# Kernel tuning notes

Hardware: AMD Instinct MI355X
Metric: run time of the kernel (lower is better)

The kernel has to match this reference:

```python
import jax, jax.numpy as jnp
import numpy as np

ANG = float(np.deg2rad(20.0))  # max rotation/shear angle (rad)
MAX_T = 6.0                    # max translation (pixels)


def _affine_mats(random, Wc, Hc):
    # Faithful to TCR.forward: note tx==ty and r==hx==hy since all use the same `random`.
    tx = (2.0 * MAX_T) * random - MAX_T
    ty = (2.0 * MAX_T) * random - MAX_T
    r = (2.0 * ANG) * random - ANG
    z = jnp.ones_like(random)          # max_z == min_z == 1.0
    hx = (2.0 * ANG) * random - ANG
    hy = (2.0 * ANG) * random - ANG
    a = hx - r
    b = hy + r
    chx, chy = jnp.cos(hx), jnp.cos(hy)
    T11 = z * jnp.cos(a) / chx
    T12 = z * jnp.sin(a) / chx
    T13 = (Wc * chx - Wc * z * jnp.cos(a) + 2 * tx * z * jnp.cos(a)
           - Hc * z * jnp.sin(a) + 2 * ty * z * jnp.sin(a)) / (2 * chx)
    T21 = z * jnp.sin(b) / chy
    T22 = z * jnp.cos(b) / chy
    T23 = (Hc * chy - Wc * z * jnp.cos(b) + 2 * ty * z * jnp.cos(b)
           - Wc * z * jnp.sin(b) + 2 * tx * z * jnp.sin(b)) / (2 * chy)
    row0 = jnp.stack([T11, T12, T13], axis=-1)
    row1 = jnp.stack([T21, T22, T23], axis=-1)
    return jnp.stack([row0, row1], axis=1)  # (B, 2, 3)


def _bilinear_sample(img, sx, sy):
    # img (B,C,H,W); sx,sy (B,H,W) source pixel coords; zeros padding (grid_sample semantics).
    B, C, H, W = img.shape
    x0f = jnp.floor(sx)
    y0f = jnp.floor(sy)
    x0 = x0f.astype(jnp.int32)
    y0 = y0f.astype(jnp.int32)
    wx = (sx - x0f)[:, None]  # (B,1,H,W)
    wy = (sy - y0f)[:, None]
    imgf = img.reshape(B, C, H * W)

    def gather(yi, xi):
        valid = (yi >= 0) & (yi < H) & (xi >= 0) & (xi < W)
        idx = jnp.clip(yi, 0, H - 1) * W + jnp.clip(xi, 0, W - 1)
        idx = jnp.broadcast_to(idx.reshape(B, 1, H * W), (B, C, H * W))
        v = jnp.take_along_axis(imgf, idx, axis=2).reshape(B, C, H, W)
        return v * valid[:, None, :, :].astype(img.dtype)

    v00 = gather(y0, x0)
    v01 = gather(y0, x0 + 1)
    v10 = gather(y0 + 1, x0)
    v11 = gather(y0 + 1, x0 + 1)
    return (v00 * (1 - wx) * (1 - wy) + v01 * wx * (1 - wy)
            + v10 * (1 - wx) * wy + v11 * wx * wy)


def _warp_affine(img, T):
    # kornia.warp_affine with align_corners=True reduces to: dst(x,y) = src(T^{-1} [x,y,1]).
    B, C, H, W = img.shape
    a, b, c = T[:, 0, 0], T[:, 0, 1], T[:, 0, 2]
    d, e, f = T[:, 1, 0], T[:, 1, 1], T[:, 1, 2]
    det = a * e - b * d
    ia, ib = e / det, -b / det
    id_, ie = -d / det, a / det
    ic = -(ia * c + ib * f)
    if_ = -(id_ * c + ie * f)
    ys, xs = jnp.meshgrid(jnp.arange(H, dtype=img.dtype),
                          jnp.arange(W, dtype=img.dtype), indexing='ij')
    bc = lambda v: v[:, None, None]  # (B,) -> (B,1,1)
    sx = bc(ia) * xs + bc(ib) * ys + bc(ic)  # (B,H,W)
    sy = bc(id_) * xs + bc(ie) * ys + bc(if_)
    return _bilinear_sample(img, sx, sy)


def setup_inputs() -> dict:
    key = jax.random.key(0)
    k1, k2 = jax.random.split(key)
    img = jax.random.normal(k1, (64, 3, 256, 256), dtype=jnp.float32)
    random = jax.random.uniform(k2, (64,), dtype=jnp.float32)
    return {"img": img, "random": random}


def reference(img, random):
    # Original uses Wc = img.shape[2], Hc = img.shape[3] (NCHW); square so equivalent.
    Wc = img.shape[2]
    Hc = img.shape[3]
    T = _affine_mats(random, float(Wc), float(Hc))
    return _warp_affine(img, T)
```

## Files before the change

kernel.cpp:

```cpp
#include <hip/hip_runtime.h>
#include <math.h>

#define BATCH 64
#define CH 3
#define IMH 256
#define IMW 256
#define HW (IMH * IMW)
#define NXCD 8

#define NRMAX 184
#define XW 36
#define XW4 9
#define NQ (NRMAX * XW4)
#define NIT 7

#define AS1 __attribute__((address_space(1)))
#define AS3 __attribute__((address_space(3)))

__device__ __forceinline__ int clampi(int v, int lo, int hi) {
    return min(max(v, lo), hi);
}

__global__ __launch_bounds__(256, 6) void TCR_52536039964687_warp(
    const float* __restrict__ img,
    const float* __restrict__ rnd,
    float* __restrict__ out) {
    __shared__ float4 lds4[NQ];
    float* lds = (float*)lds4;

    int w = blockIdx.x;
    int xcd = w & (NXCD - 1);
    unsigned t = (unsigned)w >> 3;
    unsigned islot = t / 48u;
    unsigned rem = t - islot * 48u;
    int b = ((int)islot << 3) | xcd;
    int ch = (int)(rem >> 4);
    int tile = (int)(rem & 15u);
    int X0 = (tile & 7) << 5;
    int Y0 = (tile >> 3) << 7;

    int tid = threadIdx.x;
    int dx = tid & 31;
    int qy = tid >> 5;

    const float r = rnd[b];
    const float ANG  = 0.34906585039886590f;
    const float ANG2 = 0.69813170079773179f;
    const float Wc = (float)IMH;
    const float Hc = (float)IMW;

    float tx  = 12.0f * r - 6.0f;
    float ty  = tx;
    float rho = ANG2 * r - ANG;

    float s = __sinf(rho);
    float c = __cosf(rho);
    float cb = 2.f * c * c - 1.f;
    float sb = 2.f * s * c;
    float rcb = 1.f / cb;

    float ic  = 0.5f * Wc * (1.f - c) - tx;
    float id_ = -sb * c * rcb;
    float ie  = c * rcb;
    float P   = 0.5f * (Wc * c - Wc + 2.f * tx);
    float Q   = 0.5f * (Hc * c - Wc * cb + 2.f * ty * cb - Wc * sb + 2.f * tx * sb);
    float if_ = (sb * P - Q) * rcb;

    float X0f = (float)X0, X1f = (float)(X0 + 31);
    float Y0f = (float)Y0, Y1f = (float)(Y0 + 127);
    float sxlo = fmaf(c, X0f, ic);
    int lxmin = clampi((int)floorf(sxlo), 0, IMW - 2);
    int axlo = lxmin & ~3;

    float g0 = fmaf(ie, Y0f, if_);
    float g1 = fmaf(ie, Y1f, if_);
    float syA = fmaf(id_, X0f, g0), syB = fmaf(id_, X1f, g0);
    float syC = fmaf(id_, X0f, g1), syD = fmaf(id_, X1f, g1);
    float symin = fminf(fminf(syA, syB), fminf(syC, syD));
    float symax = fmaxf(fmaxf(syA, syB), fmaxf(syC, syD));
    int rlo = clampi((int)floorf(symin), 0, IMH - 1);
    int rhi = clampi((int)floorf(symax) + 1, 0, IMH - 1);
    int NR = rhi - rlo + 1;
    int nq = NR * XW4;

    {
        const float* cbase = img + (size_t)b * CH * HW + ch * HW;
        #pragma unroll
        for (int it = 0; it < NIT; ++it) {
            int e = tid + it * 256;
            if (e < nq) {
                unsigned row = (unsigned)e / XW4;
                int q = e - (int)row * XW4;
                int gq = min(axlo + 4 * q, IMW - 4);
                const float* gp = cbase + (rlo + (int)row) * IMW + gq;
                __builtin_amdgcn_global_load_lds((const AS1 void*)gp,
                                                 (AS3 void*)&lds4[e], 16, 0, 0);
            }
        }
    }

    float fx = (float)(X0 + dx);
    float sx = fmaf(c, fx, ic);
    float x0f = floorf(sx);
    int x0 = (int)x0f;
    float wx = sx - x0f;
    int lx = clampi(x0, 0, IMW - 2);
    float wl = (x0 == lx) ? (1.f - wx) : ((x0 == lx - 1) ? wx : 0.f);
    float wh = (x0 == lx) ? wx : ((x0 == lx + 1) ? (1.f - wx) : 0.f);
    int px = lx - axlo;

    int   a01[16];
    float wy0[16], wy1[16];
    #pragma unroll
    for (int k = 0; k < 16; ++k) {
        float fy = (float)(Y0 + qy + 8 * k);
        float sy = fmaf(id_, fx, fmaf(ie, fy, if_));
        float y0f = floorf(sy);
        int y0 = (int)y0f;
        int y1 = y0 + 1;
        float wy = sy - y0f;
        wy0[k] = ((y0 >= 0) & (y0 < IMH)) ? (1.f - wy) : 0.f;
        wy1[k] = ((y1 >= 0) & (y1 < IMH)) ? wy : 0.f;
        int a0 = (clampi(y0, 0, IMH - 1) - rlo) * XW + px;
        int a1 = (clampi(y1, 0, IMH - 1) - rlo) * XW + px;
        a01[k] = a0 | (a1 << 16);
    }

    __syncthreads();

    float* obase = out + (size_t)b * CH * HW + ch * HW
                 + (Y0 + qy) * IMW + X0 + dx;
    #pragma unroll
    for (int k = 0; k < 16; ++k) {
        int a0 = a01[k] & 0xffff;
        int a1 = a01[k] >> 16;
        float l00 = lds[a0], l01 = lds[a0 + 1];
        float l10 = lds[a1], l11 = lds[a1 + 1];
        float v = (l00 * wl + l01 * wh) * wy0[k]
                + (l10 * wl + l11 * wh) * wy1[k];
        __builtin_nontemporal_store(v, obase + 8 * k * IMW);
    }
}

extern "C" void kernel_launch(void* const* d_in, const int* in_sizes, int n_in,
                              void* d_out, int out_size, void* d_ws, size_t ws_size,
                              hipStream_t stream) {
    const float* img = (const float*)d_in[0];
    const float* rnd = (const float*)d_in[1];
    float* out = (float*)d_out;
    (void)d_ws; (void)ws_size;

    hipLaunchKernelGGL(TCR_52536039964687_warp, dim3(BATCH * 16 * CH), dim3(256),
                       0, stream, img, rnd, out);
}
```

Baseline: 23.96 us.

## Switch to full-height column bands with float4 stores per thread

Each block now covers a full-height 32-column band instead of a 32x128 tile. It stages all 256 source rows of the 36-wide column window into LDS, with no computed row range, and halves the grid. Each thread produces 4 adjacent output pixels per row and writes them with a single float4 store instead of scalar nontemporal stores. This reduces per-block overhead and duplicated halo rows, at the cost of larger LDS use, lower occupancy (launch bounds 4) and more LDS loads of rows that may never be read.

```diff
diff --git a/kernel.cpp b/kernel.cpp
--- a/kernel.cpp
+++ b/kernel.cpp
@@ -8,11 +8,10 @@
 #define HW (IMH * IMW)
 #define NXCD 8
 
-#define NRMAX 184
 #define XW 36
 #define XW4 9
-#define NQ (NRMAX * XW4)
-#define NIT 7
+#define NQ (IMH * XW4)
+#define NIT 9
 
 #define AS1 __attribute__((address_space(1)))
 #define AS3 __attribute__((address_space(3)))
@@ -21,7 +20,7 @@
     return min(max(v, lo), hi);
 }
 
-__global__ __launch_bounds__(256, 6) void TCR_52536039964687_warp(
+__global__ __launch_bounds__(256, 4) void TCR_52536039964687_warp(
     const float* __restrict__ img,
     const float* __restrict__ rnd,
     float* __restrict__ out) {
@@ -31,17 +30,16 @@
     int w = blockIdx.x;
     int xcd = w & (NXCD - 1);
     unsigned t = (unsigned)w >> 3;
-    unsigned islot = t / 48u;
-    unsigned rem = t - islot * 48u;
+    unsigned islot = t / 24u;
+    unsigned rem = t - islot * 24u;
     int b = ((int)islot << 3) | xcd;
-    int ch = (int)(rem >> 4);
-    int tile = (int)(rem & 15u);
-    int X0 = (tile & 7) << 5;
-    int Y0 = (tile >> 3) << 7;
+    int ch = (int)(rem >> 3);
+    int band = (int)(rem & 7u);
+    int X0 = band << 5;
 
     int tid = threadIdx.x;
-    int dx = tid & 31;
-    int qy = tid >> 5;
+    int cg = tid & 7;
+    int qy = tid >> 3;
 
     const float r = rnd[b];
     const float ANG  = 0.34906585039886590f;
@@ -66,79 +64,66 @@
     float Q   = 0.5f * (Hc * c - Wc * cb + 2.f * ty * cb - Wc * sb + 2.f * tx * sb);
     float if_ = (sb * P - Q) * rcb;
 
-    float X0f = (float)X0, X1f = (float)(X0 + 31);
-    float Y0f = (float)Y0, Y1f = (float)(Y0 + 127);
-    float sxlo = fmaf(c, X0f, ic);
+    float sxlo = fmaf(c, (float)X0, ic);
     int lxmin = clampi((int)floorf(sxlo), 0, IMW - 2);
     int axlo = lxmin & ~3;
 
-    float g0 = fmaf(ie, Y0f, if_);
-    float g1 = fmaf(ie, Y1f, if_);
-    float syA = fmaf(id_, X0f, g0), syB = fmaf(id_, X1f, g0);
-    float syC = fmaf(id_, X0f, g1), syD = fmaf(id_, X1f, g1);
-    float symin = fminf(fminf(syA, syB), fminf(syC, syD));
-    float symax = fmaxf(fmaxf(syA, syB), fmaxf(syC, syD));
-    int rlo = clampi((int)floorf(symin), 0, IMH - 1);
-    int rhi = clampi((int)floorf(symax) + 1, 0, IMH - 1);
-    int NR = rhi - rlo + 1;
-    int nq = NR * XW4;
+    const float* cbase = img + (size_t)b * CH * HW + ch * HW;
 
-    {
-        const float* cbase = img + (size_t)b * CH * HW + ch * HW;
-        #pragma unroll
-        for (int it = 0; it < NIT; ++it) {
-            int e = tid + it * 256;
-            if (e < nq) {
-                unsigned row = (unsigned)e / XW4;
-                int q = e - (int)row * XW4;
-                int gq = min(axlo + 4 * q, IMW - 4);
-                const float* gp = cbase + (rlo + (int)row) * IMW + gq;
-                __builtin_amdgcn_global_load_lds((const AS1 void*)gp,
-                                                 (AS3 void*)&lds4[e], 16, 0, 0);
-            }
-        }
+    #pragma unroll
+    for (int it = 0; it < NIT; ++it) {
+        int e = tid + it * 256;
+        unsigned row = (unsigned)e / XW4;
+        int q = e - (int)row * XW4;
+        int gq = min(axlo + 4 * q, IMW - 4);
+        const float* gp = cbase + (int)row * IMW + gq;
+        __builtin_amdgcn_global_load_lds((const AS1 void*)gp,
+                                         (AS3 void*)&lds4[e], 16, 0, 0);
     }
 
-    float fx = (float)(X0 + dx);
-    float sx = fmaf(c, fx, ic);
-    float x0f = floorf(sx);
-    int x0 = (int)x0f;
-    float wx = sx - x0f;
-    int lx = clampi(x0, 0, IMW - 2);
-    float wl = (x0 == lx) ? (1.f - wx) : ((x0 == lx - 1) ? wx : 0.f);
-    float wh = (x0 == lx) ? wx : ((x0 == lx + 1) ? (1.f - wx) : 0.f);
-    int px = lx - axlo;
-
-    int   a01[16];
-    float wy0[16], wy1[16];
+    float wl[4], wh[4];
+    int   px[4];
+    float fxj[4];
     #pragma unroll
-    for (int k = 0; k < 16; ++k) {
-        float fy = (float)(Y0 + qy + 8 * k);
-        float sy = fmaf(id_, fx, fmaf(ie, fy, if_));
-        float y0f = floorf(sy);
-        int y0 = (int)y0f;
-        int y1 = y0 + 1;
-        float wy = sy - y0f;
-        wy0[k] = ((y0 >= 0) & (y0 < IMH)) ? (1.f - wy) : 0.f;
-        wy1[k] = ((y1 >= 0) & (y1 < IMH)) ? wy : 0.f;
-        int a0 = (clampi(y0, 0, IMH - 1) - rlo) * XW + px;
-        int a1 = (clampi(y1, 0, IMH - 1) - rlo) * XW + px;
-        a01[k] = a0 | (a1 << 16);
+    for (int j = 0; j < 4; ++j) {
+        float fx = (float)(X0 + cg * 4 + j);
+        fxj[j] = fx;
+        float sx = fmaf(c, fx, ic);
+        float x0f = floorf(sx);
+        int x0 = (int)x0f;
+        float wx = sx - x0f;
+        int lx = clampi(x0, 0, IMW - 2);
+        wl[j] = (x0 == lx) ? (1.f - wx) : ((x0 == lx - 1) ? wx : 0.f);
+        wh[j] = (x0 == lx) ? wx : ((x0 == lx + 1) ? (1.f - wx) : 0.f);
+        px[j] = lx - axlo;
     }
 
     __syncthreads();
 
-    float* obase = out + (size_t)b * CH * HW + ch * HW
-                 + (Y0 + qy) * IMW + X0 + dx;
+    float* obase = out + (size_t)b * CH * HW + ch * HW + qy * IMW + X0 + cg * 4;
+
     #pragma unroll
-    for (int k = 0; k < 16; ++k) {
-        int a0 = a01[k] & 0xffff;
-        int a1 = a01[k] >> 16;
-        float l00 = lds[a0], l01 = lds[a0 + 1];
-        float l10 = lds[a1], l11 = lds[a1 + 1];
-        float v = (l00 * wl + l01 * wh) * wy0[k]
-                + (l10 * wl + l11 * wh) * wy1[k];
-        __builtin_nontemporal_store(v, obase + 8 * k * IMW);
+    for (int rr = 0; rr < 8; ++rr) {
+        float fy = (float)(qy + 32 * rr);
+        float g = fmaf(ie, fy, if_);
+        float4 v;
+        #pragma unroll
+        for (int j = 0; j < 4; ++j) {
+            float sy = fmaf(id_, fxj[j], g);
+            float y0f = floorf(sy);
+            int y0 = (int)y0f;
+            int y1 = y0 + 1;
+            float wy = sy - y0f;
+            float wy0 = ((y0 >= 0) & (y0 < IMH)) ? (1.f - wy) : 0.f;
+            float wy1 = ((y1 >= 0) & (y1 < IMH)) ? wy : 0.f;
+            int a0 = clampi(y0, 0, IMH - 1) * XW + px[j];
+            int a1 = clampi(y1, 0, IMH - 1) * XW + px[j];
+            float l00 = lds[a0], l01 = lds[a0 + 1];
+            float l10 = lds[a1], l11 = lds[a1 + 1];
+            ((float*)&v)[j] = (l00 * wl[j] + l01 * wh[j]) * wy0
+                            + (l10 * wl[j] + l11 * wh[j]) * wy1;
+        }
+        *(float4*)(obase + rr * 32 * IMW) = v;
     }
 }
 
@@ -150,6 +135,6 @@
     float* out = (float*)d_out;
     (void)d_ws; (void)ws_size;
 
-    hipLaunchKernelGGL(TCR_52536039964687_warp, dim3(BATCH * 16 * CH), dim3(256),
+    hipLaunchKernelGGL(TCR_52536039964687_warp, dim3(BATCH * 8 * CH), dim3(256),
                        0, stream, img, rnd, out);
 }
```

Result: slower. 25.88 us (+8.0%).
